# Performance work log

Measured on AMD Instinct MI355X. Metric: run time of the kernel, lower is better.

Reference implementation:

```python
import jax, jax.numpy as jnp
import numpy as np

GH, GW, B, H, OUT = 9, 9, 1024, 256, 1


def setup_inputs() -> dict:
    key = jax.random.key(0)
    ks = jax.random.split(key, 16)
    N = GH * GW
    s3 = 1.0 / np.sqrt(3 * H)
    sH = 1.0 / np.sqrt(H)
    return {
        "x": jax.random.normal(ks[0], (B, GH, GW), jnp.float32),
        "h_ext": jax.random.normal(ks[1], (B, H), jnp.float32),
        "c_ext": jax.random.normal(ks[2], (B, H), jnp.float32),
        "grid_h": jax.random.normal(ks[3], (GH, GW, B, H), jnp.float32),
        "grid_c": jax.random.normal(ks[4], (GH, GW, B, H), jnp.float32),
        "W_hp": jax.random.normal(ks[5], (N, H, 3 * H), jnp.float32) * s3,
        "b_hp": jax.random.normal(ks[6], (N, H), jnp.float32) * s3,
        "W_cp": jax.random.normal(ks[7], (N, H, 3 * H), jnp.float32) * s3,
        "b_cp": jax.random.normal(ks[8], (N, H), jnp.float32) * s3,
        "W_ih": jax.random.normal(ks[9], (N, 4 * H, 1), jnp.float32) * sH,
        "W_hh": jax.random.normal(ks[10], (N, 4 * H, H), jnp.float32) * sH,
        "b_ih": jax.random.normal(ks[11], (N, 4 * H), jnp.float32) * sH,
        "b_hh": jax.random.normal(ks[12], (N, 4 * H), jnp.float32) * sH,
        "W_out": jax.random.normal(ks[13], (OUT, H), jnp.float32) * sH,
        "b_out": jnp.zeros((OUT,), jnp.float32),
    }


def _lstm_cell(x_cell, h0, c0, W_ih_k, W_hh_k, b_ih_k, b_hh_k):
    # x_cell: [B,1], h0/c0: [B,H]; torch LSTMCell math
    gates = x_cell @ W_ih_k.T + b_ih_k + h0 @ W_hh_k.T + b_hh_k  # [B,4H]
    i, f, g, o = jnp.split(gates, 4, axis=1)
    i, f, o = jax.nn.sigmoid(i), jax.nn.sigmoid(f), jax.nn.sigmoid(o)
    g = jnp.tanh(g)
    c = f * c0 + i * g
    h = o * jnp.tanh(c)
    return h, c


def reference(x, h_ext, c_ext, grid_h, grid_c,
              W_hp, b_hp, W_cp, b_cp,
              W_ih, W_hh, b_ih, b_hh, W_out, b_out):
    zeros = jnp.zeros((B, H), x.dtype)
    # new states, updated in raster order; left/up neighbors read NEW states
    new_h = [[None] * GW for _ in range(GH)]
    new_c = [[None] * GW for _ in range(GH)]
    for i in range(GH):
        for j in range(GW):
            k = i * GW + j
            h_prev, c_prev = grid_h[i, j], grid_c[i, j]
            if i == 0 and j == 0:
                h_left, c_left = h_ext, c_ext
            elif j > 0:
                h_left, c_left = new_h[i][j - 1], new_c[i][j - 1]
            else:
                h_left, c_left = zeros, zeros
            if i > 0:
                h_up, c_up = new_h[i - 1][j], new_c[i - 1][j]
            else:
                h_up, c_up = zeros, zeros
            comb_h = jnp.concatenate([h_left, h_up, h_prev], axis=1)  # [B,3H]
            comb_c = jnp.concatenate([c_left, c_up, c_prev], axis=1)
            ph = comb_h @ W_hp[k].T + b_hp[k]
            pc = comb_c @ W_cp[k].T + b_cp[k]
            x_cell = x[:, i, j][:, None]  # [B,1]
            h_new, c_new = _lstm_cell(x_cell, ph, pc, W_ih[k], W_hh[k], b_ih[k], b_hh[k])
            new_h[i][j], new_c[i][j] = h_new, c_new
    final_h, final_c = new_h[-1][-1], new_c[-1][-1]
    # fc_out with fc_layers_out=[0]: Linear + ReLU, then sigmoid
    out = jax.nn.sigmoid(jax.nn.relu(final_h @ W_out.T + b_out))
    gh = jnp.stack([jnp.stack(r, 0) for r in new_h], 0)
    gc = jnp.stack([jnp.stack(r, 0) for r in new_c], 0)
    return out, final_h, final_c, gh, gc
```

## Files before the change

### kernel.cpp

```cpp
#include <hip/hip_runtime.h>
#include <math.h>

#define BATCH 1024
#define HID 256
#define W3 768
#define SLOT (BATCH * HID)

typedef __bf16 bf16_t;
typedef __bf16 bf16x8 __attribute__((ext_vector_type(8)));
typedef __bf16 bf16x4 __attribute__((ext_vector_type(4)));
typedef float f32x4 __attribute__((ext_vector_type(4)));

__device__ inline bf16x8 cvt8(const float4 a, const float4 b) {
    bf16x8 r;
    r[0] = (bf16_t)a.x; r[1] = (bf16_t)a.y; r[2] = (bf16_t)a.z; r[3] = (bf16_t)a.w;
    r[4] = (bf16_t)b.x; r[5] = (bf16_t)b.y; r[6] = (bf16_t)b.z; r[7] = (bf16_t)b.w;
    return r;
}
__device__ inline bf16x4 cvt4(const float4 a) {
    bf16x4 r;
    r[0] = (bf16_t)a.x; r[1] = (bf16_t)a.y; r[2] = (bf16_t)a.z; r[3] = (bf16_t)a.w;
    return r;
}

__global__ __launch_bounds__(256) void prep_conv(
        const float* __restrict__ wcp, bf16_t* __restrict__ wcpb,
        const float* __restrict__ he, const float* __restrict__ ce,
        bf16_t* __restrict__ heb, bf16_t* __restrict__ ceb) {
    const size_t n1 = (size_t)81 * HID * W3;
    const size_t n2 = (size_t)SLOT;
    const size_t total4 = (n1 + 2 * n2) / 4;
    size_t tid = (size_t)blockIdx.x * 256 + threadIdx.x;
    const size_t nth = (size_t)gridDim.x * 256;
    for (size_t i4 = tid; i4 < total4; i4 += nth) {
        const size_t i = i4 * 4;
        const float* s; bf16_t* dst; size_t off;
        if (i < n1)            { s = wcp; dst = wcpb; off = i; }
        else if (i < n1 + n2)  { s = he;  dst = heb;  off = i - n1; }
        else                   { s = ce;  dst = ceb;  off = i - n1 - n2; }
        const float4 v = *(const float4*)(s + off);
        *(bf16x4*)(dst + off) = cvt4(v);
    }
}

__global__ __launch_bounds__(256) void gvec_kernel(
        const float* __restrict__ Whh, const float* __restrict__ bhp,
        const float* __restrict__ bih, const float* __restrict__ bhh,
        float* __restrict__ gvec) {
    const int k = blockIdx.x, t = threadIdx.x;
    __shared__ float bsm[HID];
    bsm[t] = bhp[(size_t)k * HID + t];
    __syncthreads();
    #pragma unroll
    for (int g = 0; g < 4; ++g) {
        const int n4 = g * HID + t;
        const float* wr = Whh + (size_t)k * 4 * HID * HID + (size_t)n4 * HID;
        float s = 0.f;
        for (int u = 0; u < HID; u += 4) {
            const float4 w = *(const float4*)(wr + u);
            s += w.x * bsm[u] + w.y * bsm[u + 1] + w.z * bsm[u + 2] + w.w * bsm[u + 3];
        }
        gvec[(size_t)k * 1024 + n4] = s + bih[(size_t)k * 1024 + n4]
                                        + bhh[(size_t)k * 1024 + n4];
    }
}

__global__ __launch_bounds__(256) void compose_kernel(
        const float* __restrict__ Whh, const float* __restrict__ Whp,
        bf16_t* __restrict__ CC) {
    __shared__ bf16_t As[128][40];
    __shared__ bf16_t Bs[128][40];
    const int k = blockIdx.z;
    const int t = threadIdx.x;
    const int lane = t & 63, wid = t >> 6;
    const int wm = wid & 1, wn = wid >> 1;
    const int ln = lane & 15, lh = lane >> 4;
    const int m0 = blockIdx.x * 128;
    const int by = blockIdx.y;
    const int sr = t >> 1, sq = (t & 1) * 16;
    const int g_r = sr >> 5, du_r = sr & 31;
    const float* arow = Whh + (size_t)k * 4 * HID * HID
                        + (size_t)(g_r * HID + by * 32 + du_r) * HID + sq;
    const float* wbase = Whp + (size_t)k * HID * W3;
    const int uu = t >> 3, mm0 = (t & 7) * 16;
    f32x4 acc[4][4] = {};
    for (int kb = 0; kb < 8; ++kb) {
        const float4 a0 = *(const float4*)(arow + kb * 32);
        const float4 a1 = *(const float4*)(arow + kb * 32 + 4);
        const float4 a2 = *(const float4*)(arow + kb * 32 + 8);
        const float4 a3 = *(const float4*)(arow + kb * 32 + 12);
        const float* bsrc = wbase + (size_t)(kb * 32 + uu) * W3 + m0 + mm0;
        const float4 v0 = *(const float4*)(bsrc);
        const float4 v1 = *(const float4*)(bsrc + 4);
        const float4 v2 = *(const float4*)(bsrc + 8);
        const float4 v3 = *(const float4*)(bsrc + 12);
        const bf16x8 av0 = cvt8(a0, a1), av1 = cvt8(a2, a3);
        const bf16x4 bq[4] = { cvt4(v0), cvt4(v1), cvt4(v2), cvt4(v3) };
        __syncthreads();
        *(bf16x8*)&As[sr][sq] = av0;
        *(bf16x8*)&As[sr][sq + 8] = av1;
        #pragma unroll
        for (int q = 0; q < 4; ++q)
            #pragma unroll
            for (int e = 0; e < 4; ++e)
                Bs[mm0 + q * 4 + e][uu] = bq[q][e];
        __syncthreads();
        bf16x8 af[4], bfv[4];
        #pragma unroll
        for (int mf = 0; mf < 4; ++mf)
            af[mf] = *(const bf16x8*)&As[wm * 64 + mf * 16 + ln][lh * 8];
        #pragma unroll
        for (int nf = 0; nf < 4; ++nf)
            bfv[nf] = *(const bf16x8*)&Bs[wn * 64 + nf * 16 + ln][lh * 8];
        #pragma unroll
        for (int mf = 0; mf < 4; ++mf)
            #pragma unroll
            for (int nf = 0; nf < 4; ++nf)
                acc[mf][nf] = __builtin_amdgcn_mfma_f32_16x16x32_bf16(
                    af[mf], bfv[nf], acc[mf][nf], 0, 0, 0);
    }
    bf16_t* outp = CC + (size_t)k * 1024 * W3;
    #pragma unroll
    for (int nf = 0; nf < 4; ++nf) {
        const int m = m0 + wn * 64 + nf * 16 + ln;
        #pragma unroll
        for (int mf = 0; mf < 4; ++mf)
            #pragma unroll
            for (int r = 0; r < 4; ++r) {
                const int c = by * 128 + wm * 64 + mf * 16 + lh * 4 + r;
                outp[(size_t)c * W3 + m] = (bf16_t)acc[mf][nf][r];
            }
    }
}

__global__ __launch_bounds__(256) void prevgates_kernel(
        const float* __restrict__ gridh, const float* __restrict__ gridc,
        const bf16_t* __restrict__ CC, const bf16_t* __restrict__ Wcpb,
        const float* __restrict__ gvec, const float* __restrict__ Wih,
        const float* __restrict__ bcp, const float* __restrict__ x,
        bf16_t* __restrict__ gp, bf16_t* __restrict__ pp) {
    const int k = blockIdx.z;
    __shared__ bf16_t A1[128][40];
    __shared__ bf16_t A2[128][40];
    __shared__ bf16_t B1[128][40];
    __shared__ bf16_t B2[32][40];
    const int t = threadIdx.x;
    const int lane = t & 63, wid = t >> 6;
    const int wm = wid & 1, wn = wid >> 1;
    const int ln = lane & 15, lh = lane >> 4;
    const int b0 = blockIdx.x * 128;
    const int by = blockIdx.y, u0 = by * 32;
    const int sr = t >> 1, sq = (t & 1) * 16;
    const int du2 = t >> 3, kk4 = (t & 7) * 4;

    const float* ha = gridh + (size_t)k * SLOT + (size_t)(b0 + sr) * HID + sq;
    const float* ca = gridc + (size_t)k * SLOT + (size_t)(b0 + sr) * HID + sq;
    const bf16_t* b1r = CC + (size_t)k * 1024 * W3 + (size_t)(by * 128 + sr) * W3 + 512 + sq;
    const bf16_t* b2r = Wcpb + (size_t)k * HID * W3 + (size_t)(u0 + du2) * W3 + 512 + kk4;

    f32x4 accg[4][4] = {};
    f32x4 accp[4] = {};
    for (int kb = 0; kb < 8; ++kb) {
        const float4 h0 = *(const float4*)(ha + kb * 32);
        const float4 h1 = *(const float4*)(ha + kb * 32 + 4);
        const float4 h2 = *(const float4*)(ha + kb * 32 + 8);
        const float4 h3 = *(const float4*)(ha + kb * 32 + 12);
        const float4 c0 = *(const float4*)(ca + kb * 32);
        const float4 c1 = *(const float4*)(ca + kb * 32 + 4);
        const float4 c2 = *(const float4*)(ca + kb * 32 + 8);
        const float4 c3 = *(const float4*)(ca + kb * 32 + 12);
        const bf16x8 w0 = *(const bf16x8*)(b1r + kb * 32);
        const bf16x8 w1 = *(const bf16x8*)(b1r + kb * 32 + 8);
        const bf16x4 p0 = *(const bf16x4*)(b2r + kb * 32);
        const bf16x8 hv0 = cvt8(h0, h1), hv1 = cvt8(h2, h3);
        const bf16x8 cv0 = cvt8(c0, c1), cv1 = cvt8(c2, c3);
        __syncthreads();
        *(bf16x8*)&A1[sr][sq] = hv0;  *(bf16x8*)&A1[sr][sq + 8] = hv1;
        *(bf16x8*)&A2[sr][sq] = cv0;  *(bf16x8*)&A2[sr][sq + 8] = cv1;
        *(bf16x8*)&B1[sr][sq] = w0;   *(bf16x8*)&B1[sr][sq + 8] = w1;
        *(bf16x4*)&B2[du2][kk4] = p0;
        __syncthreads();
        bf16x8 af1[4], af2[4], bf1[4], bf2;
        #pragma unroll
        for (int mf = 0; mf < 4; ++mf) {
            af1[mf] = *(const bf16x8*)&A1[wm * 64 + mf * 16 + ln][lh * 8];
            af2[mf] = *(const bf16x8*)&A2[wm * 64 + mf * 16 + ln][lh * 8];
        }
        #pragma unroll
        for (int g = 0; g < 4; ++g)
            bf1[g] = *(const bf16x8*)&B1[g * 32 + wn * 16 + ln][lh * 8];
        bf2 = *(const bf16x8*)&B2[wn * 16 + ln][lh * 8];
        #pragma unroll
        for (int mf = 0; mf < 4; ++mf) {
            #pragma unroll
            for (int g = 0; g < 4; ++g)
                accg[mf][g] = __builtin_amdgcn_mfma_f32_16x16x32_bf16(
                    af1[mf], bf1[g], accg[mf][g], 0, 0, 0);
            accp[mf] = __builtin_amdgcn_mfma_f32_16x16x32_bf16(
                af2[mf], bf2, accp[mf], 0, 0, 0);
        }
    }

    const int u = u0 + wn * 16 + ln;
    float wv[4], gv[4];
    #pragma unroll
    for (int g = 0; g < 4; ++g) {
        const int n4 = g * HID + u;
        wv[g] = Wih[(size_t)k * 1024 + n4];
        gv[g] = gvec[(size_t)k * 1024 + n4];
    }
    const float bc = bcp[(size_t)k * HID + u];
    bf16_t* gpk = gp + (size_t)k * BATCH * 1024;
    bf16_t* ppk = pp + (size_t)k * SLOT;
    #pragma unroll
    for (int mf = 0; mf < 4; ++mf)
        #pragma unroll
        for (int r = 0; r < 4; ++r) {
            const int b = b0 + wm * 64 + mf * 16 + lh * 4 + r;
            const float xv = x[(size_t)b * 81 + k];
            #pragma unroll
            for (int g = 0; g < 4; ++g)
                gpk[(size_t)b * 1024 + by * 128 + g * 32 + wn * 16 + ln] =
                    (bf16_t)(accg[mf][g][r] + gv[g] + xv * wv[g]);
            ppk[(size_t)b * HID + u] = (bf16_t)(accp[mf][r] + bc);
        }
}

struct Stage2Desc {
    const bf16_t* hs0; const bf16_t* cs0;
    const bf16_t* hs1; const bf16_t* cs1;
    const bf16_t* cc;
    const bf16_t* wcpb;
    const bf16_t* gp;
    const bf16_t* pp;
    float* gh; float* gc;
    bf16_t* ghb; bf16_t* gcb;
};
struct Stage2Args { Stage2Desc d[9]; };

__global__ __launch_bounds__(256) void stage2_kernel(Stage2Args args) {
    const Stage2Desc sd = args.d[blockIdx.z];
    __shared__ bf16_t A1[128][40];
    __shared__ bf16_t A2[128][40];
    __shared__ bf16_t B1[128][40];
    __shared__ bf16_t B2[32][40];
    const int t = threadIdx.x;
    const int lane = t & 63, wid = t >> 6;
    const int wm = wid & 1, wn = wid >> 1;
    const int ln = lane & 15, lh = lane >> 4;
    const int b0 = blockIdx.x * 128;
    const int by = blockIdx.y, u0 = by * 32;
    const int sr = t >> 1, sq = (t & 1) * 16;
    const int du2 = t >> 3, kk4 = (t & 7) * 4;

    const bf16_t* hs[2] = { sd.hs0, sd.hs1 };
    const bf16_t* cs[2] = { sd.cs0, sd.cs1 };

    f32x4 accg[4][4] = {};
    f32x4 accp[4] = {};

    for (int s = 0; s < 2; ++s) {
        if (!hs[s]) continue;
        const int ko = s * 256;
        const bf16_t* ha = hs[s] + (size_t)(b0 + sr) * HID + sq;
        const bf16_t* ca = cs[s] + (size_t)(b0 + sr) * HID + sq;
        const bf16_t* b1r = sd.cc + (size_t)(by * 128 + sr) * W3 + ko + sq;
        const bf16_t* b2r = sd.wcpb + (size_t)(u0 + du2) * W3 + ko + kk4;
        for (int kb = 0; kb < 8; ++kb) {
            const bf16x8 h0 = *(const bf16x8*)(ha + kb * 32);
            const bf16x8 h1 = *(const bf16x8*)(ha + kb * 32 + 8);
            const bf16x8 c0 = *(const bf16x8*)(ca + kb * 32);
            const bf16x8 c1 = *(const bf16x8*)(ca + kb * 32 + 8);
            const bf16x8 w0 = *(const bf16x8*)(b1r + kb * 32);
            const bf16x8 w1 = *(const bf16x8*)(b1r + kb * 32 + 8);
            const bf16x4 p0 = *(const bf16x4*)(b2r + kb * 32);
            __syncthreads();
            *(bf16x8*)&A1[sr][sq] = h0;  *(bf16x8*)&A1[sr][sq + 8] = h1;
            *(bf16x8*)&A2[sr][sq] = c0;  *(bf16x8*)&A2[sr][sq + 8] = c1;
            *(bf16x8*)&B1[sr][sq] = w0;  *(bf16x8*)&B1[sr][sq + 8] = w1;
            *(bf16x4*)&B2[du2][kk4] = p0;
            __syncthreads();
            bf16x8 af1[4], af2[4], bf1[4], bf2;
            #pragma unroll
            for (int mf = 0; mf < 4; ++mf) {
                af1[mf] = *(const bf16x8*)&A1[wm * 64 + mf * 16 + ln][lh * 8];
                af2[mf] = *(const bf16x8*)&A2[wm * 64 + mf * 16 + ln][lh * 8];
            }
            #pragma unroll
            for (int g = 0; g < 4; ++g)
                bf1[g] = *(const bf16x8*)&B1[g * 32 + wn * 16 + ln][lh * 8];
            bf2 = *(const bf16x8*)&B2[wn * 16 + ln][lh * 8];
            #pragma unroll
            for (int mf = 0; mf < 4; ++mf) {
                #pragma unroll
                for (int g = 0; g < 4; ++g)
                    accg[mf][g] = __builtin_amdgcn_mfma_f32_16x16x32_bf16(
                        af1[mf], bf1[g], accg[mf][g], 0, 0, 0);
                accp[mf] = __builtin_amdgcn_mfma_f32_16x16x32_bf16(
                    af2[mf], bf2, accp[mf], 0, 0, 0);
            }
        }
    }

    const int u = u0 + wn * 16 + ln;
    #pragma unroll
    for (int mf = 0; mf < 4; ++mf)
        #pragma unroll
        for (int r = 0; r < 4; ++r) {
            const int b = b0 + wm * 64 + mf * 16 + lh * 4 + r;
            const bf16_t* gpr = sd.gp + (size_t)b * 1024 + by * 128 + wn * 16 + ln;
            const float gi = accg[mf][0][r] + (float)gpr[0];
            const float gf = accg[mf][1][r] + (float)gpr[32];
            const float gg = accg[mf][2][r] + (float)gpr[64];
            const float go = accg[mf][3][r] + (float)gpr[96];
            const float pc = accp[mf][r] + (float)sd.pp[(size_t)b * HID + u];
            const float i_ = 1.f / (1.f + expf(-gi));
            const float f_ = 1.f / (1.f + expf(-gf));
            const float o_ = 1.f / (1.f + expf(-go));
            const float g_ = tanhf(gg);
            const float cn = f_ * pc + i_ * g_;
            const float hn = o_ * tanhf(cn);
            sd.gh[(size_t)b * HID + u] = hn;
            sd.gc[(size_t)b * HID + u] = cn;
            sd.ghb[(size_t)b * HID + u] = (bf16_t)hn;
            sd.gcb[(size_t)b * HID + u] = (bf16_t)cn;
        }
}

__global__ __launch_bounds__(256) void final_kernel(
        const float* __restrict__ gh88, const float* __restrict__ gc88,
        const float* __restrict__ Wout, const float* __restrict__ bout,
        float* __restrict__ out, float* __restrict__ fh, float* __restrict__ fc) {
    const int tid = blockIdx.x * blockDim.x + threadIdx.x;
    const int nth = gridDim.x * blockDim.x;
    for (int idx = tid; idx < BATCH * HID; idx += nth) {
        fh[idx] = gh88[idx];
        fc[idx] = gc88[idx];
    }
    if (tid < BATCH) {
        float s = bout[0];
        for (int k = 0; k < HID; ++k) s += gh88[(size_t)tid * HID + k] * Wout[k];
        s = fmaxf(s, 0.f);
        out[tid] = 1.f / (1.f + expf(-s));
    }
}

template<bool ATOMIC>
__device__ __forceinline__ void proj_core(
        const float* __restrict__ src, const float* __restrict__ W, int koff,
        const float* __restrict__ bias, float* __restrict__ out,
        bf16_t (*Asm)[40], bf16_t (*Bsm)[40]) {
    const int t = threadIdx.x;
    const int lane = t & 63, wid = t >> 6;
    const int wm = wid & 1, wn = wid >> 1;
    const int ln = lane & 15, lh = lane >> 4;
    const int b0 = blockIdx.x * 128, n0 = blockIdx.y * 128;
    const int sr = t >> 1, sq = (t & 1) * 16;
    const float* arow = src + (size_t)(b0 + sr) * HID + sq;
    const float* wrow = W + (size_t)(n0 + sr) * W3 + koff + sq;
    f32x4 acc[4][4] = {};
    for (int kb = 0; kb < 8; ++kb) {
        const float4 a0 = *(const float4*)(arow + kb * 32);
        const float4 a1 = *(const float4*)(arow + kb * 32 + 4);
        const float4 a2 = *(const float4*)(arow + kb * 32 + 8);
        const float4 a3 = *(const float4*)(arow + kb * 32 + 12);
        const float4 w0 = *(const float4*)(wrow + kb * 32);
        const float4 w1 = *(const float4*)(wrow + kb * 32 + 4);
        const float4 w2 = *(const float4*)(wrow + kb * 32 + 8);
        const float4 w3 = *(const float4*)(wrow + kb * 32 + 12);
        const bf16x8 av0 = cvt8(a0, a1), av1 = cvt8(a2, a3);
        const bf16x8 bv0 = cvt8(w0, w1), bv1 = cvt8(w2, w3);
        __syncthreads();
        *(bf16x8*)&Asm[sr][sq] = av0;
        *(bf16x8*)&Asm[sr][sq + 8] = av1;
        *(bf16x8*)&Bsm[sr][sq] = bv0;
        *(bf16x8*)&Bsm[sr][sq + 8] = bv1;
        __syncthreads();
        bf16x8 af[4], bfv[4];
        #pragma unroll
        for (int mf = 0; mf < 4; ++mf)
            af[mf] = *(const bf16x8*)&Asm[wm * 64 + mf * 16 + ln][lh * 8];
        #pragma unroll
        for (int nf = 0; nf < 4; ++nf)
            bfv[nf] = *(const bf16x8*)&Bsm[wn * 64 + nf * 16 + ln][lh * 8];
        #pragma unroll
        for (int mf = 0; mf < 4; ++mf)
            #pragma unroll
            for (int nf = 0; nf < 4; ++nf)
                acc[mf][nf] = __builtin_amdgcn_mfma_f32_16x16x32_bf16(
                    af[mf], bfv[nf], acc[mf][nf], 0, 0, 0);
    }
    #pragma unroll
    for (int nf = 0; nf < 4; ++nf) {
        const int n = n0 + wn * 64 + nf * 16 + ln;
        const float bn = ATOMIC ? 0.f : bias[n];
        #pragma unroll
        for (int mf = 0; mf < 4; ++mf)
            #pragma unroll
            for (int r = 0; r < 4; ++r) {
                const int b = b0 + wm * 64 + mf * 16 + lh * 4 + r;
                if (ATOMIC)
                    unsafeAtomicAdd(out + (size_t)b * HID + n, acc[mf][nf][r]);
                else
                    out[(size_t)b * HID + n] = acc[mf][nf][r] + bn;
            }
    }
}

struct SegDesc { const float* src; const float* W; const float* bias; float* out; int koff; };
struct SegArgs { SegDesc d[36]; };

__global__ __launch_bounds__(256) void projseg_kernel(SegArgs a) {
    __shared__ bf16_t As[128][40];
    __shared__ bf16_t Bs[128][40];
    const SegDesc d = a.d[blockIdx.z];
    if (d.bias) proj_core<false>(d.src, d.W, d.koff, d.bias, d.out, As, Bs);
    else        proj_core<true>(d.src, d.W, d.koff, nullptr, d.out, As, Bs);
}

struct CellDesc {
    const float* ph; const float* pc;
    const float* Whh; const float* Wih; const float* bih; const float* bhh;
    const float* xcol;
    float* gh; float* gc;
};
struct CellBatchArgs { CellDesc d[9]; };

__global__ __launch_bounds__(256) void cell_kernel(CellBatchArgs args) {
    const CellDesc cd = args.d[blockIdx.z];
    __shared__ bf16_t Psm[128][40];
    __shared__ bf16_t Wsm[128][40];
    const int t = threadIdx.x;
    const int lane = t & 63, wid = t >> 6;
    const int wm = wid & 1, wn = wid >> 1;
    const int ln = lane & 15, lh = lane >> 4;
    const int b0 = blockIdx.x * 128;
    const int u0 = blockIdx.y * 32;
    const int sr = t >> 1, sq = (t & 1) * 16;
    const float* prow = cd.ph + (size_t)(b0 + sr) * HID + sq;
    const int cg = sr >> 5, cdu = sr & 31;
    const float* wrow = cd.Whh + (size_t)(cg * HID + u0 + cdu) * HID + sq;
    f32x4 acc[4][4] = {};
    for (int kb = 0; kb < 8; ++kb) {
        const float4 p0 = *(const float4*)(prow + kb * 32);
        const float4 p1 = *(const float4*)(prow + kb * 32 + 4);
        const float4 p2 = *(const float4*)(prow + kb * 32 + 8);
        const float4 p3 = *(const float4*)(prow + kb * 32 + 12);
        const float4 w0 = *(const float4*)(wrow + kb * 32);
        const float4 w1 = *(const float4*)(wrow + kb * 32 + 4);
        const float4 w2 = *(const float4*)(wrow + kb * 32 + 8);
        const float4 w3 = *(const float4*)(wrow + kb * 32 + 12);
        const bf16x8 pv0 = cvt8(p0, p1), pv1 = cvt8(p2, p3);
        const bf16x8 wv0 = cvt8(w0, w1), wv1 = cvt8(w2, w3);
        __syncthreads();
        *(bf16x8*)&Psm[sr][sq] = pv0;
        *(bf16x8*)&Psm[sr][sq + 8] = pv1;
        *(bf16x8*)&Wsm[sr][sq] = wv0;
        *(bf16x8*)&Wsm[sr][sq + 8] = wv1;
        __syncthreads();
        bf16x8 af[4], bfr[4];
        #pragma unroll
        for (int mf = 0; mf < 4; ++mf)
            af[mf] = *(const bf16x8*)&Psm[wm * 64 + mf * 16 + ln][lh * 8];
        #pragma unroll
        for (int g = 0; g < 4; ++g)
            bfr[g] = *(const bf16x8*)&Wsm[g * 32 + wn * 16 + ln][lh * 8];
        #pragma unroll
        for (int mf = 0; mf < 4; ++mf)
            #pragma unroll
            for (int g = 0; g < 4; ++g)
                acc[mf][g] = __builtin_amdgcn_mfma_f32_16x16x32_bf16(
                    af[mf], bfr[g], acc[mf][g], 0, 0, 0);
    }
    const int u = u0 + wn * 16 + ln;
    float wih[4], bsum[4];
    #pragma unroll
    for (int g = 0; g < 4; ++g) {
        const int n = g * HID + u;
        wih[g] = cd.Wih[n];
        bsum[g] = cd.bih[n] + cd.bhh[n];
    }
    #pragma unroll
    for (int mf = 0; mf < 4; ++mf)
        #pragma unroll
        for (int r = 0; r < 4; ++r) {
            const int b = b0 + wm * 64 + mf * 16 + lh * 4 + r;
            const float xv = cd.xcol[(size_t)b * 81];
            const float gi = acc[mf][0][r] + xv * wih[0] + bsum[0];
            const float gf = acc[mf][1][r] + xv * wih[1] + bsum[1];
            const float gg = acc[mf][2][r] + xv * wih[2] + bsum[2];
            const float go = acc[mf][3][r] + xv * wih[3] + bsum[3];
            const float i_ = 1.f / (1.f + expf(-gi));
            const float f_ = 1.f / (1.f + expf(-gf));
            const float o_ = 1.f / (1.f + expf(-go));
            const float g_ = tanhf(gg);
            const float c0 = cd.pc[(size_t)b * HID + u];
            const float cn = f_ * c0 + i_ * g_;
            const float hn = o_ * tanhf(cn);
            cd.gh[(size_t)b * HID + u] = hn;
            cd.gc[(size_t)b * HID + u] = cn;
        }
}

extern "C" void kernel_launch(void* const* d_in, const int* in_sizes, int n_in,
                              void* d_out, int out_size, void* d_ws, size_t ws_size,
                              hipStream_t stream) {
    const float* x      = (const float*)d_in[0];
    const float* h_ext  = (const float*)d_in[1];
    const float* c_ext  = (const float*)d_in[2];
    const float* grid_h = (const float*)d_in[3];
    const float* grid_c = (const float*)d_in[4];
    const float* W_hp   = (const float*)d_in[5];
    const float* b_hp   = (const float*)d_in[6];
    const float* W_cp   = (const float*)d_in[7];
    const float* b_cp   = (const float*)d_in[8];
    const float* W_ih   = (const float*)d_in[9];
    const float* W_hh   = (const float*)d_in[10];
    const float* b_ih   = (const float*)d_in[11];
    const float* b_hh   = (const float*)d_in[12];
    const float* W_out  = (const float*)d_in[13];
    const float* b_out  = (const float*)d_in[14];

    float* out = (float*)d_out;
    float* fh  = out + BATCH * 1;
    float* fc  = fh + SLOT;
    float* gh  = fc + SLOT;
    float* gc  = gh + (size_t)81 * SLOT;

    const size_t cc_b  = (size_t)81 * 1024 * W3 * 2;
    const size_t wcp_b = (size_t)81 * HID * W3 * 2;
    const size_t gp_b  = (size_t)81 * BATCH * 1024 * 2;
    const size_t pp_b  = (size_t)81 * SLOT * 2;
    const size_t st_b  = (size_t)81 * SLOT * 2;
    const size_t ext_b = (size_t)SLOT * 2;
    const size_t gv_b  = (size_t)81 * 1024 * 4;
    const size_t need = cc_b + wcp_b + gp_b + pp_b + 2 * st_b + 2 * ext_b + gv_b;

    if (ws_size >= need) {
        char* p = (char*)d_ws;
        bf16_t* CC   = (bf16_t*)p; p += cc_b;
        bf16_t* Wcpb = (bf16_t*)p; p += wcp_b;
        bf16_t* GP   = (bf16_t*)p; p += gp_b;
        bf16_t* PP   = (bf16_t*)p; p += pp_b;
        bf16_t* GHB  = (bf16_t*)p; p += st_b;
        bf16_t* GCB  = (bf16_t*)p; p += st_b;
        bf16_t* HEB  = (bf16_t*)p; p += ext_b;
        bf16_t* CEB  = (bf16_t*)p; p += ext_b;
        float*  gvec = (float*)p;

        prep_conv<<<dim3(2048), 256, 0, stream>>>(W_cp, Wcpb, h_ext, c_ext, HEB, CEB);
        gvec_kernel<<<dim3(81), 256, 0, stream>>>(W_hh, b_hp, b_ih, b_hh, gvec);
        compose_kernel<<<dim3(6, 8, 81), 256, 0, stream>>>(W_hh, W_hp, CC);
        prevgates_kernel<<<dim3(8, 8, 81), 256, 0, stream>>>(
            grid_h, grid_c, CC, Wcpb, gvec, W_ih, b_cp, x, GP, PP);

        for (int d = 0; d <= 16; ++d) {
            const int i_lo = d > 8 ? d - 8 : 0;
            const int i_hi = d < 8 ? d : 8;
            const int nc = i_hi - i_lo + 1;
            Stage2Args sa{};
            for (int s = 0; s < nc; ++s) {
                const int i = i_lo + s, j = d - i;
                const int k = i * 9 + j;
                const bf16_t *hl = nullptr, *cl = nullptr, *hu = nullptr, *cu = nullptr;
                if (i == 0 && j == 0)      { hl = HEB; cl = CEB; }
                else if (j > 0)            { hl = GHB + (size_t)(k - 1) * SLOT;
                                             cl = GCB + (size_t)(k - 1) * SLOT; }
                if (i > 0)                 { hu = GHB + (size_t)(k - 9) * SLOT;
                                             cu = GCB + (size_t)(k - 9) * SLOT; }
                sa.d[s] = { hl, cl, hu, cu,
                            CC + (size_t)k * 1024 * W3,
                            Wcpb + (size_t)k * HID * W3,
                            GP + (size_t)k * BATCH * 1024,
                            PP + (size_t)k * SLOT,
                            gh + (size_t)k * SLOT, gc + (size_t)k * SLOT,
                            GHB + (size_t)k * SLOT, GCB + (size_t)k * SLOT };
            }
            stage2_kernel<<<dim3(8, 8, nc), 256, 0, stream>>>(sa);
        }
    } else {
        float* ws = (float*)d_ws;
        for (int d = 0; d <= 16; ++d) {
            const int i_lo = d > 8 ? d - 8 : 0;
            const int i_hi = d < 8 ? d : 8;
            const int nc = i_hi - i_lo + 1;
            SegArgs base{}, inc{};
            CellBatchArgs ca{};
            int nb = 0, ni = 0;
            for (int s = 0; s < nc; ++s) {
                const int i = i_lo + s, j = d - i;
                const int k = i * 9 + j;
                float* oh = ws + (size_t)(2 * s) * SLOT;
                float* oc = oh + SLOT;
                const float* Wh = W_hp + (size_t)k * HID * W3;
                const float* Wc = W_cp + (size_t)k * HID * W3;
                base.d[nb++] = { grid_h + (size_t)k * SLOT, Wh, b_hp + (size_t)k * HID, oh, 512 };
                base.d[nb++] = { grid_c + (size_t)k * SLOT, Wc, b_cp + (size_t)k * HID, oc, 512 };
                if (i == 0 && j == 0) {
                    inc.d[ni++] = { h_ext, Wh, nullptr, oh, 0 };
                    inc.d[ni++] = { c_ext, Wc, nullptr, oc, 0 };
                } else if (j > 0) {
                    inc.d[ni++] = { gh + (size_t)(k - 1) * SLOT, Wh, nullptr, oh, 0 };
                    inc.d[ni++] = { gc + (size_t)(k - 1) * SLOT, Wc, nullptr, oc, 0 };
                }
                if (i > 0) {
                    inc.d[ni++] = { gh + (size_t)(k - 9) * SLOT, Wh, nullptr, oh, 256 };
                    inc.d[ni++] = { gc + (size_t)(k - 9) * SLOT, Wc, nullptr, oc, 256 };
                }
                ca.d[s] = { oh, oc,
                            W_hh + (size_t)k * 4 * HID * HID,
                            W_ih + (size_t)k * 4 * HID,
                            b_ih + (size_t)k * 4 * HID,
                            b_hh + (size_t)k * 4 * HID,
                            x + i * 9 + j,
                            gh + (size_t)k * SLOT,
                            gc + (size_t)k * SLOT };
            }
            projseg_kernel<<<dim3(8, 2, nb), 256, 0, stream>>>(base);
            projseg_kernel<<<dim3(8, 2, ni), 256, 0, stream>>>(inc);
            cell_kernel<<<dim3(8, 8, nc), 256, 0, stream>>>(ca);
        }
    }
    final_kernel<<<dim3(64), 256, 0, stream>>>(
        gh + (size_t)80 * SLOT, gc + (size_t)80 * SLOT,
        W_out, b_out, out, fh, fc);
}
```

Before: 1.124 ms.

## Drop LDS staging, load MFMA fragments directly, swizzle blocks across XCDs

Removes shared-memory staging and barriers in the compose, prevgates and stage2 GEMMs, so each lane loads its MFMA fragments straight from global memory. A pre-transposed bf16 copy of W_hp feeds compose. The gate and peephole intermediates are stored in a per-block fragment-native layout so they can be read back with vector loads. The bf16 shadow copies of the new states are dropped, and stage2 reads fp32 states and converts them itself. Blocks are flattened to 1D and remapped so consecutive work lands on the same XCD. The cost is uncoalesced, strided global fragment loads with no LDS reuse, plus an extra transpose kernel.

```diff
diff --git a/kernel.cpp b/kernel.cpp
--- a/kernel.cpp
+++ b/kernel.cpp
@@ -23,23 +23,39 @@
     return r;
 }
 
-__global__ __launch_bounds__(256) void prep_conv(
-        const float* __restrict__ wcp, bf16_t* __restrict__ wcpb,
-        const float* __restrict__ he, const float* __restrict__ ce,
-        bf16_t* __restrict__ heb, bf16_t* __restrict__ ceb) {
-    const size_t n1 = (size_t)81 * HID * W3;
-    const size_t n2 = (size_t)SLOT;
-    const size_t total4 = (n1 + 2 * n2) / 4;
-    size_t tid = (size_t)blockIdx.x * 256 + threadIdx.x;
+__device__ inline int swz_work(int bid, int N) {
+    const int xcd = bid & 7, idx = bid >> 3;
+    const int q = N >> 3, r = N & 7;
+    return (xcd < r ? xcd * (q + 1) : r * (q + 1) + (xcd - r) * q) + idx;
+}
+
+__global__ __launch_bounds__(256) void wcp_conv(
+        const float* __restrict__ wcp, bf16_t* __restrict__ wcpb) {
+    const size_t n4 = (size_t)81 * HID * W3 / 4;
+    size_t i = (size_t)blockIdx.x * 256 + threadIdx.x;
     const size_t nth = (size_t)gridDim.x * 256;
-    for (size_t i4 = tid; i4 < total4; i4 += nth) {
-        const size_t i = i4 * 4;
-        const float* s; bf16_t* dst; size_t off;
-        if (i < n1)            { s = wcp; dst = wcpb; off = i; }
-        else if (i < n1 + n2)  { s = he;  dst = heb;  off = i - n1; }
-        else                   { s = ce;  dst = ceb;  off = i - n1 - n2; }
-        const float4 v = *(const float4*)(s + off);
-        *(bf16x4*)(dst + off) = cvt4(v);
+    for (; i < n4; i += nth) {
+        const float4 v = *(const float4*)(wcp + i * 4);
+        *(bf16x4*)(wcpb + i * 4) = cvt4(v);
+    }
+}
+
+__global__ __launch_bounds__(256) void whp_t_kernel(
+        const float* __restrict__ whp, bf16_t* __restrict__ whpT) {
+    const int k = blockIdx.z;
+    const int m0 = blockIdx.x * 64, u0 = blockIdx.y * 64;
+    const int t = threadIdx.x;
+    const int tm = t & 63, tg = t >> 6;
+    const float* src = whp + (size_t)k * HID * W3;
+    bf16_t* dst = whpT + (size_t)k * W3 * HID;
+    #pragma unroll
+    for (int c = 0; c < 2; ++c) {
+        const int ub = u0 + (tg + c * 4) * 8;
+        bf16x8 v;
+        #pragma unroll
+        for (int i = 0; i < 8; ++i)
+            v[i] = (bf16_t)src[(size_t)(ub + i) * W3 + m0 + tm];
+        *(bf16x8*)(dst + (size_t)(m0 + tm) * HID + ub) = v;
     }
 }
 
@@ -66,52 +82,43 @@
 }
 
 __global__ __launch_bounds__(256) void compose_kernel(
-        const float* __restrict__ Whh, const float* __restrict__ Whp,
+        const float* __restrict__ Whh, const bf16_t* __restrict__ WhpT,
         bf16_t* __restrict__ CC) {
-    __shared__ bf16_t As[128][40];
-    __shared__ bf16_t Bs[128][40];
-    const int k = blockIdx.z;
+    const int work = swz_work(blockIdx.x, gridDim.x);
+    const int k = work / 48, inner = work % 48;
+    const int mt = inner % 6, by = inner / 6;
+    const int m0 = mt * 128;
     const int t = threadIdx.x;
     const int lane = t & 63, wid = t >> 6;
     const int wm = wid & 1, wn = wid >> 1;
     const int ln = lane & 15, lh = lane >> 4;
-    const int m0 = blockIdx.x * 128;
-    const int by = blockIdx.y;
-    const int sr = t >> 1, sq = (t & 1) * 16;
-    const int g_r = sr >> 5, du_r = sr & 31;
-    const float* arow = Whh + (size_t)k * 4 * HID * HID
-                        + (size_t)(g_r * HID + by * 32 + du_r) * HID + sq;
-    const float* wbase = Whp + (size_t)k * HID * W3;
-    const int uu = t >> 3, mm0 = (t & 7) * 16;
+    const float* abase = Whh + (size_t)k * 1024 * HID;
+    const bf16_t* bbase = WhpT + (size_t)k * W3 * HID;
+    const float* arow[4];
+    #pragma unroll
+    for (int mf = 0; mf < 4; ++mf) {
+        const int cl = wm * 64 + mf * 16 + ln;
+        const int n4 = (cl >> 5) * HID + by * 32 + (cl & 31);
+        arow[mf] = abase + (size_t)n4 * HID + lh * 8;
+    }
+    const bf16_t* brow[4];
+    #pragma unroll
+    for (int nf = 0; nf < 4; ++nf)
+        brow[nf] = bbase + (size_t)(m0 + wn * 64 + nf * 16 + ln) * HID + lh * 8;
+
     f32x4 acc[4][4] = {};
+    #pragma unroll 2
     for (int kb = 0; kb < 8; ++kb) {
-        const float4 a0 = *(const float4*)(arow + kb * 32);
-        const float4 a1 = *(const float4*)(arow + kb * 32 + 4);
-        const float4 a2 = *(const float4*)(arow + kb * 32 + 8);
-        const float4 a3 = *(const float4*)(arow + kb * 32 + 12);
-        const float* bsrc = wbase + (size_t)(kb * 32 + uu) * W3 + m0 + mm0;
-        const float4 v0 = *(const float4*)(bsrc);
-        const float4 v1 = *(const float4*)(bsrc + 4);
-        const float4 v2 = *(const float4*)(bsrc + 8);
-        const float4 v3 = *(const float4*)(bsrc + 12);
-        const bf16x8 av0 = cvt8(a0, a1), av1 = cvt8(a2, a3);
-        const bf16x4 bq[4] = { cvt4(v0), cvt4(v1), cvt4(v2), cvt4(v3) };
-        __syncthreads();
-        *(bf16x8*)&As[sr][sq] = av0;
-        *(bf16x8*)&As[sr][sq + 8] = av1;
-        #pragma unroll
-        for (int q = 0; q < 4; ++q)
-            #pragma unroll
-            for (int e = 0; e < 4; ++e)
-                Bs[mm0 + q * 4 + e][uu] = bq[q][e];
-        __syncthreads();
         bf16x8 af[4], bfv[4];
         #pragma unroll
-        for (int mf = 0; mf < 4; ++mf)
-            af[mf] = *(const bf16x8*)&As[wm * 64 + mf * 16 + ln][lh * 8];
+        for (int mf = 0; mf < 4; ++mf) {
+            const float4 a0 = *(const float4*)(arow[mf] + kb * 32);
+            const float4 a1 = *(const float4*)(arow[mf] + kb * 32 + 4);
+            af[mf] = cvt8(a0, a1);
+        }
         #pragma unroll
         for (int nf = 0; nf < 4; ++nf)
-            bfv[nf] = *(const bf16x8*)&Bs[wn * 64 + nf * 16 + ln][lh * 8];
+            bfv[nf] = *(const bf16x8*)(brow[nf] + kb * 32);
         #pragma unroll
         for (int mf = 0; mf < 4; ++mf)
             #pragma unroll
@@ -124,12 +131,12 @@
     for (int nf = 0; nf < 4; ++nf) {
         const int m = m0 + wn * 64 + nf * 16 + ln;
         #pragma unroll
-        for (int mf = 0; mf < 4; ++mf)
-            #pragma unroll
-            for (int r = 0; r < 4; ++r) {
-                const int c = by * 128 + wm * 64 + mf * 16 + lh * 4 + r;
-                outp[(size_t)c * W3 + m] = (bf16_t)acc[mf][nf][r];
-            }
+        for (int mf = 0; mf < 4; ++mf) {
+            const int cb = by * 128 + wm * 64 + mf * 16 + lh * 4;
+            #pragma unroll
+            for (int r = 0; r < 4; ++r)
+                outp[(size_t)(cb + r) * W3 + m] = (bf16_t)acc[mf][nf][r];
+        }
     }
 }
 
@@ -138,66 +145,59 @@
         const bf16_t* __restrict__ CC, const bf16_t* __restrict__ Wcpb,
         const float* __restrict__ gvec, const float* __restrict__ Wih,
         const float* __restrict__ bcp, const float* __restrict__ x,
-        bf16_t* __restrict__ gp, bf16_t* __restrict__ pp) {
-    const int k = blockIdx.z;
-    __shared__ bf16_t A1[128][40];
-    __shared__ bf16_t A2[128][40];
-    __shared__ bf16_t B1[128][40];
-    __shared__ bf16_t B2[32][40];
+        bf16_t* __restrict__ GP, bf16_t* __restrict__ PP) {
+    const int work = swz_work(blockIdx.x, gridDim.x);
+    const int k = work >> 6, inner = work & 63;
+    const int bx = inner & 7, by = inner >> 3;
     const int t = threadIdx.x;
     const int lane = t & 63, wid = t >> 6;
     const int wm = wid & 1, wn = wid >> 1;
     const int ln = lane & 15, lh = lane >> 4;
-    const int b0 = blockIdx.x * 128;
-    const int by = blockIdx.y, u0 = by * 32;
-    const int sr = t >> 1, sq = (t & 1) * 16;
-    const int du2 = t >> 3, kk4 = (t & 7) * 4;
-
-    const float* ha = gridh + (size_t)k * SLOT + (size_t)(b0 + sr) * HID + sq;
-    const float* ca = gridc + (size_t)k * SLOT + (size_t)(b0 + sr) * HID + sq;
-    const bf16_t* b1r = CC + (size_t)k * 1024 * W3 + (size_t)(by * 128 + sr) * W3 + 512 + sq;
-    const bf16_t* b2r = Wcpb + (size_t)k * HID * W3 + (size_t)(u0 + du2) * W3 + 512 + kk4;
+    const int b0 = bx * 128, u0 = by * 32;
+
+    const float* hb = gridh + (size_t)k * SLOT;
+    const float* cb = gridc + (size_t)k * SLOT;
+    const float* ha[4]; const float* ca[4];
+    #pragma unroll
+    for (int mf = 0; mf < 4; ++mf) {
+        const int b = b0 + wm * 64 + mf * 16 + ln;
+        ha[mf] = hb + (size_t)b * HID + lh * 8;
+        ca[mf] = cb + (size_t)b * HID + lh * 8;
+    }
+    const bf16_t* ccb = CC + (size_t)k * 1024 * W3;
+    const bf16_t* b1[4];
+    #pragma unroll
+    for (int g = 0; g < 4; ++g)
+        b1[g] = ccb + (size_t)(by * 128 + g * 32 + wn * 16 + ln) * W3 + 512 + lh * 8;
+    const bf16_t* b2 = Wcpb + (size_t)k * HID * W3
+                       + (size_t)(u0 + wn * 16 + ln) * W3 + 512 + lh * 8;
 
     f32x4 accg[4][4] = {};
     f32x4 accp[4] = {};
+    #pragma unroll 2
     for (int kb = 0; kb < 8; ++kb) {
-        const float4 h0 = *(const float4*)(ha + kb * 32);
-        const float4 h1 = *(const float4*)(ha + kb * 32 + 4);
-        const float4 h2 = *(const float4*)(ha + kb * 32 + 8);
-        const float4 h3 = *(const float4*)(ha + kb * 32 + 12);
-        const float4 c0 = *(const float4*)(ca + kb * 32);
-        const float4 c1 = *(const float4*)(ca + kb * 32 + 4);
-        const float4 c2 = *(const float4*)(ca + kb * 32 + 8);
-        const float4 c3 = *(const float4*)(ca + kb * 32 + 12);
-        const bf16x8 w0 = *(const bf16x8*)(b1r + kb * 32);
-        const bf16x8 w1 = *(const bf16x8*)(b1r + kb * 32 + 8);
-        const bf16x4 p0 = *(const bf16x4*)(b2r + kb * 32);
-        const bf16x8 hv0 = cvt8(h0, h1), hv1 = cvt8(h2, h3);
-        const bf16x8 cv0 = cvt8(c0, c1), cv1 = cvt8(c2, c3);
-        __syncthreads();
-        *(bf16x8*)&A1[sr][sq] = hv0;  *(bf16x8*)&A1[sr][sq + 8] = hv1;
-        *(bf16x8*)&A2[sr][sq] = cv0;  *(bf16x8*)&A2[sr][sq + 8] = cv1;
-        *(bf16x8*)&B1[sr][sq] = w0;   *(bf16x8*)&B1[sr][sq + 8] = w1;
-        *(bf16x4*)&B2[du2][kk4] = p0;
-        __syncthreads();
-        bf16x8 af1[4], af2[4], bf1[4], bf2;
+        bf16x8 afh[4], afc[4], bfg[4], bfp;
         #pragma unroll
         for (int mf = 0; mf < 4; ++mf) {
-            af1[mf] = *(const bf16x8*)&A1[wm * 64 + mf * 16 + ln][lh * 8];
-            af2[mf] = *(const bf16x8*)&A2[wm * 64 + mf * 16 + ln][lh * 8];
+            const float4 h0 = *(const float4*)(ha[mf] + kb * 32);
+            const float4 h1 = *(const float4*)(ha[mf] + kb * 32 + 4);
+            const float4 c0 = *(const float4*)(ca[mf] + kb * 32);
+            const float4 c1 = *(const float4*)(ca[mf] + kb * 32 + 4);
+            afh[mf] = cvt8(h0, h1);
+            afc[mf] = cvt8(c0, c1);
         }
         #pragma unroll
         for (int g = 0; g < 4; ++g)
-            bf1[g] = *(const bf16x8*)&B1[g * 32 + wn * 16 + ln][lh * 8];
-        bf2 = *(const bf16x8*)&B2[wn * 16 + ln][lh * 8];
+            bfg[g] = *(const bf16x8*)(b1[g] + kb * 32);
+        bfp = *(const bf16x8*)(b2 + kb * 32);
         #pragma unroll
         for (int mf = 0; mf < 4; ++mf) {
             #pragma unroll
             for (int g = 0; g < 4; ++g)
                 accg[mf][g] = __builtin_amdgcn_mfma_f32_16x16x32_bf16(
-                    af1[mf], bf1[g], accg[mf][g], 0, 0, 0);
+                    afh[mf], bfg[g], accg[mf][g], 0, 0, 0);
             accp[mf] = __builtin_amdgcn_mfma_f32_16x16x32_bf16(
-                af2[mf], bf2, accp[mf], 0, 0, 0);
+                afc[mf], bfp, accp[mf], 0, 0, 0);
         }
     }
 
@@ -210,121 +210,150 @@
         gv[g] = gvec[(size_t)k * 1024 + n4];
     }
     const float bc = bcp[(size_t)k * HID + u];
-    bf16_t* gpk = gp + (size_t)k * BATCH * 1024;
-    bf16_t* ppk = pp + (size_t)k * SLOT;
-    #pragma unroll
-    for (int mf = 0; mf < 4; ++mf)
-        #pragma unroll
-        for (int r = 0; r < 4; ++r) {
-            const int b = b0 + wm * 64 + mf * 16 + lh * 4 + r;
-            const float xv = x[(size_t)b * 81 + k];
-            #pragma unroll
-            for (int g = 0; g < 4; ++g)
-                gpk[(size_t)b * 1024 + by * 128 + g * 32 + wn * 16 + ln] =
-                    (bf16_t)(accg[mf][g][r] + gv[g] + xv * wv[g]);
-            ppk[(size_t)b * HID + u] = (bf16_t)(accp[mf][r] + bc);
-        }
+    const int blk = by * 8 + bx;
+    bf16_t* gpb = GP + (size_t)k * (BATCH * 1024) + (size_t)blk * 16384;
+    bf16_t* ppb = PP + (size_t)k * SLOT + (size_t)blk * 4096;
+    #pragma unroll
+    for (int mf = 0; mf < 4; ++mf) {
+        #pragma unroll
+        for (int rp = 0; rp < 2; ++rp) {
+            bf16x8 v;
+            #pragma unroll
+            for (int a = 0; a < 2; ++a) {
+                const int r = rp * 2 + a;
+                const int b = b0 + wm * 64 + mf * 16 + lh * 4 + r;
+                const float xv = x[(size_t)b * 81 + k];
+                #pragma unroll
+                for (int g = 0; g < 4; ++g)
+                    v[a * 4 + g] = (bf16_t)(accg[mf][g][r] + gv[g] + xv * wv[g]);
+            }
+            *(bf16x8*)(gpb + (size_t)(mf * 2 + rp) * 2048 + t * 8) = v;
+        }
+    }
+    #pragma unroll
+    for (int j = 0; j < 2; ++j) {
+        bf16x8 v;
+        #pragma unroll
+        for (int h2 = 0; h2 < 2; ++h2) {
+            const int mf = j * 2 + h2;
+            #pragma unroll
+            for (int r = 0; r < 4; ++r)
+                v[h2 * 4 + r] = (bf16_t)(accp[mf][r] + bc);
+        }
+        *(bf16x8*)(ppb + (size_t)j * 2048 + t * 8) = v;
+    }
 }
 
 struct Stage2Desc {
-    const bf16_t* hs0; const bf16_t* cs0;
-    const bf16_t* hs1; const bf16_t* cs1;
-    const bf16_t* cc;
-    const bf16_t* wcpb;
-    const bf16_t* gp;
-    const bf16_t* pp;
+    const float* hs0; const float* cs0;
+    const float* hs1; const float* cs1;
+    const bf16_t* cc; const bf16_t* wcpb;
+    const bf16_t* gp; const bf16_t* pp;
     float* gh; float* gc;
-    bf16_t* ghb; bf16_t* gcb;
 };
 struct Stage2Args { Stage2Desc d[9]; };
 
 __global__ __launch_bounds__(256) void stage2_kernel(Stage2Args args) {
-    const Stage2Desc sd = args.d[blockIdx.z];
-    __shared__ bf16_t A1[128][40];
-    __shared__ bf16_t A2[128][40];
-    __shared__ bf16_t B1[128][40];
-    __shared__ bf16_t B2[32][40];
+    const int work = swz_work(blockIdx.x, gridDim.x);
+    const int cell = work >> 6, inner = work & 63;
+    const Stage2Desc sd = args.d[cell];
+    const int bx = inner & 7, by = inner >> 3;
     const int t = threadIdx.x;
     const int lane = t & 63, wid = t >> 6;
     const int wm = wid & 1, wn = wid >> 1;
     const int ln = lane & 15, lh = lane >> 4;
-    const int b0 = blockIdx.x * 128;
-    const int by = blockIdx.y, u0 = by * 32;
-    const int sr = t >> 1, sq = (t & 1) * 16;
-    const int du2 = t >> 3, kk4 = (t & 7) * 4;
-
-    const bf16_t* hs[2] = { sd.hs0, sd.hs1 };
-    const bf16_t* cs[2] = { sd.cs0, sd.cs1 };
+    const int b0 = bx * 128, u0 = by * 32;
 
     f32x4 accg[4][4] = {};
     f32x4 accp[4] = {};
-
+    const float* hseg[2] = { sd.hs0, sd.hs1 };
+    const float* cseg[2] = { sd.cs0, sd.cs1 };
+
+    #pragma unroll
     for (int s = 0; s < 2; ++s) {
-        if (!hs[s]) continue;
+        const float* hp = hseg[s];
+        if (!hp) continue;
+        const float* cp = cseg[s];
         const int ko = s * 256;
-        const bf16_t* ha = hs[s] + (size_t)(b0 + sr) * HID + sq;
-        const bf16_t* ca = cs[s] + (size_t)(b0 + sr) * HID + sq;
-        const bf16_t* b1r = sd.cc + (size_t)(by * 128 + sr) * W3 + ko + sq;
-        const bf16_t* b2r = sd.wcpb + (size_t)(u0 + du2) * W3 + ko + kk4;
+        const float* ha[4]; const float* ca[4];
+        #pragma unroll
+        for (int mf = 0; mf < 4; ++mf) {
+            const int b = b0 + wm * 64 + mf * 16 + ln;
+            ha[mf] = hp + (size_t)b * HID + lh * 8;
+            ca[mf] = cp + (size_t)b * HID + lh * 8;
+        }
+        const bf16_t* b1[4];
+        #pragma unroll
+        for (int g = 0; g < 4; ++g)
+            b1[g] = sd.cc + (size_t)(by * 128 + g * 32 + wn * 16 + ln) * W3 + ko + lh * 8;
+        const bf16_t* b2 = sd.wcpb + (size_t)(u0 + wn * 16 + ln) * W3 + ko + lh * 8;
+        #pragma unroll 2
         for (int kb = 0; kb < 8; ++kb) {
-            const bf16x8 h0 = *(const bf16x8*)(ha + kb * 32);
-            const bf16x8 h1 = *(const bf16x8*)(ha + kb * 32 + 8);
-            const bf16x8 c0 = *(const bf16x8*)(ca + kb * 32);
-            const bf16x8 c1 = *(const bf16x8*)(ca + kb * 32 + 8);
-            const bf16x8 w0 = *(const bf16x8*)(b1r + kb * 32);
-            const bf16x8 w1 = *(const bf16x8*)(b1r + kb * 32 + 8);
-            const bf16x4 p0 = *(const bf16x4*)(b2r + kb * 32);
-            __syncthreads();
-            *(bf16x8*)&A1[sr][sq] = h0;  *(bf16x8*)&A1[sr][sq + 8] = h1;
-            *(bf16x8*)&A2[sr][sq] = c0;  *(bf16x8*)&A2[sr][sq + 8] = c1;
-            *(bf16x8*)&B1[sr][sq] = w0;  *(bf16x8*)&B1[sr][sq + 8] = w1;
-            *(bf16x4*)&B2[du2][kk4] = p0;
-            __syncthreads();
-            bf16x8 af1[4], af2[4], bf1[4], bf2;
+            bf16x8 afh[4], afc[4], bfg[4], bfp;
             #pragma unroll
             for (int mf = 0; mf < 4; ++mf) {
-                af1[mf] = *(const bf16x8*)&A1[wm * 64 + mf * 16 + ln][lh * 8];
-                af2[mf] = *(const bf16x8*)&A2[wm * 64 + mf * 16 + ln][lh * 8];
+                const float4 h0 = *(const float4*)(ha[mf] + kb * 32);
+                const float4 h1 = *(const float4*)(ha[mf] + kb * 32 + 4);
+                const float4 c0 = *(const float4*)(ca[mf] + kb * 32);
+                const float4 c1 = *(const float4*)(ca[mf] + kb * 32 + 4);
+                afh[mf] = cvt8(h0, h1);
+                afc[mf] = cvt8(c0, c1);
             }
             #pragma unroll
             for (int g = 0; g < 4; ++g)
-                bf1[g] = *(const bf16x8*)&B1[g * 32 + wn * 16 + ln][lh * 8];
-            bf2 = *(const bf16x8*)&B2[wn * 16 + ln][lh * 8];
+                bfg[g] = *(const bf16x8*)(b1[g] + kb * 32);
+            bfp = *(const bf16x8*)(b2 + kb * 32);
             #pragma unroll
             for (int mf = 0; mf < 4; ++mf) {
                 #pragma unroll
                 for (int g = 0; g < 4; ++g)
                     accg[mf][g] = __builtin_amdgcn_mfma_f32_16x16x32_bf16(
-                        af1[mf], bf1[g], accg[mf][g], 0, 0, 0);
+                        afh[mf], bfg[g], accg[mf][g], 0, 0, 0);
                 accp[mf] = __builtin_amdgcn_mfma_f32_16x16x32_bf16(
-                    af2[mf], bf2, accp[mf], 0, 0, 0);
+                    afc[mf], bfp, accp[mf], 0, 0, 0);
             }
         }
     }
 
     const int u = u0 + wn * 16 + ln;
-    #pragma unroll
-    for (int mf = 0; mf < 4; ++mf)
-        #pragma unroll
-        for (int r = 0; r < 4; ++r) {
-            const int b = b0 + wm * 64 + mf * 16 + lh * 4 + r;
-            const bf16_t* gpr = sd.gp + (size_t)b * 1024 + by * 128 + wn * 16 + ln;
-            const float gi = accg[mf][0][r] + (float)gpr[0];
-            const float gf = accg[mf][1][r] + (float)gpr[32];
-            const float gg = accg[mf][2][r] + (float)gpr[64];
-            const float go = accg[mf][3][r] + (float)gpr[96];
-            const float pc = accp[mf][r] + (float)sd.pp[(size_t)b * HID + u];
-            const float i_ = 1.f / (1.f + expf(-gi));
-            const float f_ = 1.f / (1.f + expf(-gf));
-            const float o_ = 1.f / (1.f + expf(-go));
-            const float g_ = tanhf(gg);
-            const float cn = f_ * pc + i_ * g_;
-            const float hn = o_ * tanhf(cn);
-            sd.gh[(size_t)b * HID + u] = hn;
-            sd.gc[(size_t)b * HID + u] = cn;
-            sd.ghb[(size_t)b * HID + u] = (bf16_t)hn;
-            sd.gcb[(size_t)b * HID + u] = (bf16_t)cn;
-        }
+    const int blk = by * 8 + bx;
+    const bf16_t* gpb = sd.gp + (size_t)blk * 16384;
+    const bf16_t* ppb = sd.pp + (size_t)blk * 4096;
+    float pcv[4][4];
+    #pragma unroll
+    for (int j = 0; j < 2; ++j) {
+        const bf16x8 v = *(const bf16x8*)(ppb + (size_t)j * 2048 + t * 8);
+        #pragma unroll
+        for (int h2 = 0; h2 < 2; ++h2)
+            #pragma unroll
+            for (int r = 0; r < 4; ++r)
+                pcv[j * 2 + h2][r] = accp[j * 2 + h2][r] + (float)v[h2 * 4 + r];
+    }
+    #pragma unroll
+    for (int mf = 0; mf < 4; ++mf) {
+        #pragma unroll
+        for (int rp = 0; rp < 2; ++rp) {
+            const bf16x8 v = *(const bf16x8*)(gpb + (size_t)(mf * 2 + rp) * 2048 + t * 8);
+            #pragma unroll
+            for (int a = 0; a < 2; ++a) {
+                const int r = rp * 2 + a;
+                const int b = b0 + wm * 64 + mf * 16 + lh * 4 + r;
+                const float gi = accg[mf][0][r] + (float)v[a * 4 + 0];
+                const float gf = accg[mf][1][r] + (float)v[a * 4 + 1];
+                const float gg = accg[mf][2][r] + (float)v[a * 4 + 2];
+                const float go = accg[mf][3][r] + (float)v[a * 4 + 3];
+                const float pc = pcv[mf][r];
+                const float i_ = 1.f / (1.f + expf(-gi));
+                const float f_ = 1.f / (1.f + expf(-gf));
+                const float o_ = 1.f / (1.f + expf(-go));
+                const float g_ = tanhf(gg);
+                const float cn = f_ * pc + i_ * g_;
+                const float hn = o_ * tanhf(cn);
+                sd.gh[(size_t)b * HID + u] = hn;
+                sd.gc[(size_t)b * HID + u] = cn;
+            }
+        }
+    }
 }
 
 __global__ __launch_bounds__(256) void final_kernel(
@@ -527,31 +556,28 @@
     float* gh  = fc + SLOT;
     float* gc  = gh + (size_t)81 * SLOT;
 
+    const size_t wt_b  = (size_t)81 * W3 * HID * 2;
+    const size_t wcp_b = (size_t)81 * HID * W3 * 2;
     const size_t cc_b  = (size_t)81 * 1024 * W3 * 2;
-    const size_t wcp_b = (size_t)81 * HID * W3 * 2;
     const size_t gp_b  = (size_t)81 * BATCH * 1024 * 2;
     const size_t pp_b  = (size_t)81 * SLOT * 2;
-    const size_t st_b  = (size_t)81 * SLOT * 2;
-    const size_t ext_b = (size_t)SLOT * 2;
     const size_t gv_b  = (size_t)81 * 1024 * 4;
-    const size_t need = cc_b + wcp_b + gp_b + pp_b + 2 * st_b + 2 * ext_b + gv_b;
+    const size_t need = wt_b + wcp_b + cc_b + gp_b + pp_b + gv_b;
 
     if (ws_size >= need) {
         char* p = (char*)d_ws;
+        bf16_t* WhpT = (bf16_t*)p; p += wt_b;
+        bf16_t* Wcpb = (bf16_t*)p; p += wcp_b;
         bf16_t* CC   = (bf16_t*)p; p += cc_b;
-        bf16_t* Wcpb = (bf16_t*)p; p += wcp_b;
         bf16_t* GP   = (bf16_t*)p; p += gp_b;
         bf16_t* PP   = (bf16_t*)p; p += pp_b;
-        bf16_t* GHB  = (bf16_t*)p; p += st_b;
-        bf16_t* GCB  = (bf16_t*)p; p += st_b;
-        bf16_t* HEB  = (bf16_t*)p; p += ext_b;
-        bf16_t* CEB  = (bf16_t*)p; p += ext_b;
         float*  gvec = (float*)p;
 
-        prep_conv<<<dim3(2048), 256, 0, stream>>>(W_cp, Wcpb, h_ext, c_ext, HEB, CEB);
+        wcp_conv<<<dim3(2048), 256, 0, stream>>>(W_cp, Wcpb);
+        whp_t_kernel<<<dim3(12, 4, 81), 256, 0, stream>>>(W_hp, WhpT);
         gvec_kernel<<<dim3(81), 256, 0, stream>>>(W_hh, b_hp, b_ih, b_hh, gvec);
-        compose_kernel<<<dim3(6, 8, 81), 256, 0, stream>>>(W_hh, W_hp, CC);
-        prevgates_kernel<<<dim3(8, 8, 81), 256, 0, stream>>>(
+        compose_kernel<<<dim3(81 * 48), 256, 0, stream>>>(W_hh, WhpT, CC);
+        prevgates_kernel<<<dim3(81 * 64), 256, 0, stream>>>(
             grid_h, grid_c, CC, Wcpb, gvec, W_ih, b_cp, x, GP, PP);
 
         for (int d = 0; d <= 16; ++d) {
@@ -562,21 +588,20 @@
             for (int s = 0; s < nc; ++s) {
                 const int i = i_lo + s, j = d - i;
                 const int k = i * 9 + j;
-                const bf16_t *hl = nullptr, *cl = nullptr, *hu = nullptr, *cu = nullptr;
-                if (i == 0 && j == 0)      { hl = HEB; cl = CEB; }
-                else if (j > 0)            { hl = GHB + (size_t)(k - 1) * SLOT;
-                                             cl = GCB + (size_t)(k - 1) * SLOT; }
-                if (i > 0)                 { hu = GHB + (size_t)(k - 9) * SLOT;
-                                             cu = GCB + (size_t)(k - 9) * SLOT; }
+                const float *hl = nullptr, *cl = nullptr, *hu = nullptr, *cu = nullptr;
+                if (i == 0 && j == 0)      { hl = h_ext; cl = c_ext; }
+                else if (j > 0)            { hl = gh + (size_t)(k - 1) * SLOT;
+                                             cl = gc + (size_t)(k - 1) * SLOT; }
+                if (i > 0)                 { hu = gh + (size_t)(k - 9) * SLOT;
+                                             cu = gc + (size_t)(k - 9) * SLOT; }
                 sa.d[s] = { hl, cl, hu, cu,
                             CC + (size_t)k * 1024 * W3,
                             Wcpb + (size_t)k * HID * W3,
                             GP + (size_t)k * BATCH * 1024,
                             PP + (size_t)k * SLOT,
-                            gh + (size_t)k * SLOT, gc + (size_t)k * SLOT,
-                            GHB + (size_t)k * SLOT, GCB + (size_t)k * SLOT };
+                            gh + (size_t)k * SLOT, gc + (size_t)k * SLOT };
             }
-            stage2_kernel<<<dim3(8, 8, nc), 256, 0, stream>>>(sa);
+            stage2_kernel<<<dim3(nc * 64), 256, 0, stream>>>(sa);
         }
     } else {
         float* ws = (float*)d_ws;
```

New measurement: 2.081 ms. 1.85x slower.
